# Performance work log

Measured on AMD Instinct MI355X. Metric: run time of the kernel, lower is better.

The kernel has to match this reference:

```python
import jax, jax.numpy as jnp
import numpy as np

LOG_STD2 = float(np.log(0.001))  # matches nn.init posterior_W_u/v fill, unused: params are random here


def _mvg_layer(x, M, u, v, eps):
    # append ones column (bias trick): [B, in] -> [B, in+1]
    x1 = jnp.concatenate([x, jnp.ones((x.shape[0], 1), x.dtype)], axis=1)
    # W = M + diag(exp(.5u)) @ eps @ diag(exp(.5v))  ==  M + row/col scaled eps
    W = M + jnp.exp(0.5 * u)[:, None] * eps * jnp.exp(0.5 * v)[None, :]
    return x1 @ W


def setup_inputs() -> dict:
    key = jax.random.key(0)
    ks = jax.random.split(key, 17)
    dims = [(2049, 4096), (4097, 4096), (4097, 4096), (4097, 2048)]
    inp = {"x": jax.random.normal(ks[0], (8192, 2048), dtype=jnp.float32)}
    ki = 1
    for i, (fin, fout) in enumerate(dims):
        inp[f"M{i}"] = jax.random.normal(ks[ki], (fin, fout), dtype=jnp.float32) * 0.001; ki += 1
        inp[f"u{i}"] = jax.random.normal(ks[ki], (fin,), dtype=jnp.float32) + LOG_STD2; ki += 1
        inp[f"v{i}"] = jax.random.normal(ks[ki], (fout,), dtype=jnp.float32) + LOG_STD2; ki += 1
        inp[f"eps{i}"] = jax.random.normal(ks[ki], (fin, fout), dtype=jnp.float32); ki += 1
    return inp


def reference(x, M0, u0, v0, eps0, M1, u1, v1, eps1, M2, u2, v2, eps2, M3, u3, v3, eps3):
    h = _mvg_layer(x, M0, u0, v0, eps0)
    h = _mvg_layer(jax.nn.relu(h), M1, u1, v1, eps1)
    h = _mvg_layer(jax.nn.relu(h), M2, u2, v2, eps2)
    h = _mvg_layer(jax.nn.relu(h), M3, u3, v3, eps3)
    return h
```

## Files before the change

kernel.cpp:

```cpp
#include <hip/hip_runtime.h>
#include <cstdint>
#include <cstddef>

typedef __bf16 bf16_t;
typedef __attribute__((ext_vector_type(8))) __bf16 bf16x8;
typedef __attribute__((ext_vector_type(4))) __bf16 bf16x4;
typedef __attribute__((ext_vector_type(4))) float floatx4;

__device__ __forceinline__ void cp16(const void* g, void* l) {
  __builtin_amdgcn_global_load_lds(
      (const __attribute__((address_space(1))) void*)(uintptr_t)g,
      (__attribute__((address_space(3))) void*)(uintptr_t)l, 16, 0, 0);
}

__global__ void cvt_to_bf16(const float4* __restrict__ in,
                            bf16x4* __restrict__ out, int n4) {
  int i = blockIdx.x * 256 + threadIdx.x;
  if (i < n4) {
    float4 f = in[i];
    bf16x4 o;
    o[0] = (bf16_t)f.x; o[1] = (bf16_t)f.y; o[2] = (bf16_t)f.z; o[3] = (bf16_t)f.w;
    out[i] = o;
  }
}

__global__ void prep_wt(const float* __restrict__ M, const float* __restrict__ u,
                        const float* __restrict__ v, const float* __restrict__ eps,
                        bf16_t* __restrict__ Wt, int K, int N) {
  __shared__ float tile[32][33];
  const int nb = blockIdx.x * 32, kb = blockIdx.y * 32;
  const int tx = threadIdx.x, ty = threadIdx.y;
  const float sv = __expf(0.5f * v[nb + tx]);
#pragma unroll
  for (int r = 0; r < 4; ++r) {
    const int k = kb + ty + 8 * r;
    const float su = __expf(0.5f * u[k]);
    const size_t idx = (size_t)k * N + nb + tx;
    tile[ty + 8 * r][tx] = M[idx] + su * eps[idx] * sv;
  }
  __syncthreads();
#pragma unroll
  for (int r = 0; r < 4; ++r) {
    const int n = nb + ty + 8 * r;
    Wt[(size_t)n * K + kb + tx] = (bf16_t)tile[tx][ty + 8 * r];
  }
}

__global__ void prep_bias(const float* __restrict__ M, const float* __restrict__ u,
                          const float* __restrict__ v, const float* __restrict__ eps,
                          float* __restrict__ bias, int K, int N) {
  int n = blockIdx.x * 256 + threadIdx.x;
  if (n < N) {
    const size_t idx = (size_t)K * N + n;
    bias[n] = M[idx] + __expf(0.5f * u[K]) * eps[idx] * __expf(0.5f * v[n]);
  }
}

template <int EPI>
__global__ __launch_bounds__(256, 2) void gemm_bt(
    const bf16_t* __restrict__ A, const bf16_t* __restrict__ Bt,
    const float* __restrict__ bias, void* __restrict__ Cout, int N, int K) {
  __shared__ bf16_t As[128 * 32];
  __shared__ bf16_t Bs[128 * 32];

  const int tid = threadIdx.x;
  const int lane = tid & 63;
  const int wave = tid >> 6;
  const int wm = (wave >> 1) * 64;
  const int wn = (wave & 1) * 64;
  const int bm = blockIdx.y * 128;
  const int bn = blockIdx.x * 128;

  const int srow = tid >> 2;
  const int scol = (tid & 3) * 8;
  const bf16_t* aG0 = A + (size_t)(bm + srow) * K + scol;
  const bf16_t* aG1 = aG0 + (size_t)64 * K;
  const bf16_t* bG0 = Bt + (size_t)(bn + srow) * K + scol;
  const bf16_t* bG1 = bG0 + (size_t)64 * K;
  char* aL0 = (char*)As + tid * 16;
  char* aL1 = aL0 + 4096;
  char* bL0 = (char*)Bs + tid * 16;
  char* bL1 = bL0 + 4096;

  floatx4 acc[4][4] = {};

  const int mRow = wm + (lane & 15);
  const int nRow = wn + (lane & 15);
  const int kq = lane >> 4;

  for (int k0 = 0; k0 < K; k0 += 32) {
    cp16(aG0 + k0, aL0);
    cp16(aG1 + k0, aL1);
    cp16(bG0 + k0, bL0);
    cp16(bG1 + k0, bL1);
    __syncthreads();

    const bf16x8* As8 = (const bf16x8*)As;
    const bf16x8* Bs8 = (const bf16x8*)Bs;
    bf16x8 af[4], bfr[4];
#pragma unroll
    for (int i = 0; i < 4; ++i) af[i] = As8[(mRow + i * 16) * 4 + kq];
#pragma unroll
    for (int j = 0; j < 4; ++j) bfr[j] = Bs8[(nRow + j * 16) * 4 + kq];
#pragma unroll
    for (int i = 0; i < 4; ++i)
#pragma unroll
      for (int j = 0; j < 4; ++j)
        acc[i][j] = __builtin_amdgcn_mfma_f32_16x16x32_bf16(af[i], bfr[j],
                                                            acc[i][j], 0, 0, 0);
    __syncthreads();
  }

  const int col = bn + wn + (lane & 15);
  const int row0 = bm + wm + kq * 4;
#pragma unroll
  for (int j = 0; j < 4; ++j) {
    const float bj = bias[col + j * 16];
#pragma unroll
    for (int i = 0; i < 4; ++i) {
#pragma unroll
      for (int r = 0; r < 4; ++r) {
        float v = acc[i][j][r] + bj;
        const size_t idx = (size_t)(row0 + i * 16 + r) * N + (col + j * 16);
        if (EPI == 0) {
          v = v > 0.f ? v : 0.f;
          ((bf16_t*)Cout)[idx] = (bf16_t)v;
        } else {
          ((float*)Cout)[idx] = v;
        }
      }
    }
  }
}

extern "C" void kernel_launch(void* const* d_in, const int* in_sizes, int n_in,
                              void* d_out, int out_size, void* d_ws, size_t ws_size,
                              hipStream_t stream) {
  const float* x = (const float*)d_in[0];
  const float *Mm[4], *uu[4], *vv[4], *ee[4];
  for (int i = 0; i < 4; ++i) {
    Mm[i] = (const float*)d_in[1 + 4 * i];
    uu[i] = (const float*)d_in[2 + 4 * i];
    vv[i] = (const float*)d_in[3 + 4 * i];
    ee[i] = (const float*)d_in[4 + 4 * i];
  }

  char* ws = (char*)d_ws;
  bf16_t* Wt0 = (bf16_t*)ws;
  bf16_t* Wt1 = (bf16_t*)(ws + 16777216);
  bf16_t* Wt2 = (bf16_t*)(ws + 16777216 + 33554432);
  bf16_t* Wt3 = (bf16_t*)(ws + 16777216 + 2u * 33554432);
  char* bptr = ws + 2u * 16777216 + 2u * 33554432;
  float* bias0 = (float*)(bptr);
  float* bias1 = (float*)(bptr + 16384);
  float* bias2 = (float*)(bptr + 32768);
  float* bias3 = (float*)(bptr + 49152);
  char* act = bptr + 65536;
  bf16_t* hA = (bf16_t*)act;
  bf16_t* hB = (bf16_t*)(act + 67108864);
  bf16_t* xb = (bf16_t*)d_out;

  cvt_to_bf16<<<16384, 256, 0, stream>>>((const float4*)x, (bf16x4*)xb,
                                         8192 * 2048 / 4);
  prep_wt<<<dim3(4096 / 32, 2048 / 32), dim3(32, 8), 0, stream>>>(
      Mm[0], uu[0], vv[0], ee[0], Wt0, 2048, 4096);
  prep_wt<<<dim3(4096 / 32, 4096 / 32), dim3(32, 8), 0, stream>>>(
      Mm[1], uu[1], vv[1], ee[1], Wt1, 4096, 4096);
  prep_wt<<<dim3(4096 / 32, 4096 / 32), dim3(32, 8), 0, stream>>>(
      Mm[2], uu[2], vv[2], ee[2], Wt2, 4096, 4096);
  prep_wt<<<dim3(2048 / 32, 4096 / 32), dim3(32, 8), 0, stream>>>(
      Mm[3], uu[3], vv[3], ee[3], Wt3, 4096, 2048);
  prep_bias<<<16, 256, 0, stream>>>(Mm[0], uu[0], vv[0], ee[0], bias0, 2048, 4096);
  prep_bias<<<16, 256, 0, stream>>>(Mm[1], uu[1], vv[1], ee[1], bias1, 4096, 4096);
  prep_bias<<<16, 256, 0, stream>>>(Mm[2], uu[2], vv[2], ee[2], bias2, 4096, 4096);
  prep_bias<<<8, 256, 0, stream>>>(Mm[3], uu[3], vv[3], ee[3], bias3, 4096, 2048);

  gemm_bt<0><<<dim3(32, 64), 256, 0, stream>>>(xb, Wt0, bias0, hA, 4096, 2048);
  gemm_bt<0><<<dim3(32, 64), 256, 0, stream>>>(hA, Wt1, bias1, hB, 4096, 4096);
  gemm_bt<0><<<dim3(32, 64), 256, 0, stream>>>(hB, Wt2, bias2, hA, 4096, 4096);
  gemm_bt<1><<<dim3(16, 64), 256, 0, stream>>>(hA, Wt3, bias3, d_out, 2048, 4096);
}
```

Before: 1.317 ms.

## Replace 128x128 GEMM with 256x256 double-buffered pipelined bf16 MFMA kernel

Replaces the simple single-buffered 128x128 tile GEMM with a 512-thread 256x256 tile kernel. It uses a 64-deep K step, double-buffered dynamic LDS (128 KB), and XOR-swizzled LDS layout to avoid bank conflicts. Global-to-LDS prefetch of the next tiles is interleaved with MFMA phases using sched barriers and setprio, and a block-id remap improves L2 locality. This removes the per-iteration full sync stalls and low arithmetic intensity of the old kernel, at the cost of high register and LDS use that limits occupancy, plus intricate waitcnt logic that is easy to get wrong.

```diff
diff --git a/kernel.cpp b/kernel.cpp
--- a/kernel.cpp
+++ b/kernel.cpp
@@ -11,6 +11,12 @@
   __builtin_amdgcn_global_load_lds(
       (const __attribute__((address_space(1))) void*)(uintptr_t)g,
       (__attribute__((address_space(3))) void*)(uintptr_t)l, 16, 0, 0);
+}
+
+__device__ __forceinline__ void stage_half(const bf16_t* p, int K, char* dst,
+                                           int tid) {
+  cp16(p, dst + tid * 16);
+  cp16(p + (size_t)128 * K, dst + 8192 + tid * 16);
 }
 
 __global__ void cvt_to_bf16(const float4* __restrict__ in,
@@ -56,72 +62,160 @@
   }
 }
 
+template <int CURB>
+__device__ __forceinline__ void ktile(int t, int NT, int K,
+                                      const bf16_t* gA, const bf16_t* gB,
+                                      char* lds, int tid, int aoff0, int boff0,
+                                      floatx4 (&acc)[8][4]) {
+  constexpr int curO = CURB * 65536;
+  constexpr int nxtO = (CURB ^ 1) * 65536;
+  bf16x8 af[4], bb[4];
+
+#pragma unroll
+  for (int m = 0; m < 4; ++m)
+    af[m] = *(const bf16x8*)(lds + curO + aoff0 + m * 1024);
+#pragma unroll
+  for (int n = 0; n < 4; ++n)
+    bb[n] = *(const bf16x8*)(lds + curO + 32768 + boff0 + n * 1024);
+  if (t + 1 < NT)
+    stage_half(gA + (size_t)(t + 1) * 64 + 32, K, lds + nxtO + 16384, tid);
+  __builtin_amdgcn_s_barrier();
+  asm volatile("s_waitcnt lgkmcnt(0)" ::: "memory");
+  __builtin_amdgcn_sched_barrier(0);
+  __builtin_amdgcn_s_setprio(1);
+#pragma unroll
+  for (int m = 0; m < 4; ++m)
+#pragma unroll
+    for (int n = 0; n < 4; ++n)
+      acc[m][n] = __builtin_amdgcn_mfma_f32_16x16x32_bf16(af[m], bb[n],
+                                                          acc[m][n], 0, 0, 0);
+  __builtin_amdgcn_s_setprio(0);
+  __builtin_amdgcn_sched_barrier(0);
+  __builtin_amdgcn_s_barrier();
+
+#pragma unroll
+  for (int m = 0; m < 4; ++m)
+    af[m] = *(const bf16x8*)(lds + curO + aoff0 + (m + 4) * 1024);
+  if (t + 1 < NT)
+    stage_half(gB + (size_t)(t + 1) * 64 + 32, K, lds + nxtO + 49152, tid);
+  __builtin_amdgcn_s_barrier();
+  asm volatile("s_waitcnt lgkmcnt(0)" ::: "memory");
+  __builtin_amdgcn_sched_barrier(0);
+  __builtin_amdgcn_s_setprio(1);
+#pragma unroll
+  for (int m = 0; m < 4; ++m)
+#pragma unroll
+    for (int n = 0; n < 4; ++n)
+      acc[m + 4][n] = __builtin_amdgcn_mfma_f32_16x16x32_bf16(af[m], bb[n],
+                                                              acc[m + 4][n], 0, 0, 0);
+  __builtin_amdgcn_s_setprio(0);
+  __builtin_amdgcn_sched_barrier(0);
+  __builtin_amdgcn_s_barrier();
+
+#pragma unroll
+  for (int m = 0; m < 4; ++m)
+    af[m] = *(const bf16x8*)(lds + curO + 16384 + aoff0 + m * 1024);
+#pragma unroll
+  for (int n = 0; n < 4; ++n)
+    bb[n] = *(const bf16x8*)(lds + curO + 49152 + boff0 + n * 1024);
+  if (t + 2 < NT)
+    stage_half(gA + (size_t)(t + 2) * 64, K, lds + curO, tid);
+  __builtin_amdgcn_s_barrier();
+  asm volatile("s_waitcnt lgkmcnt(0)" ::: "memory");
+  __builtin_amdgcn_sched_barrier(0);
+  __builtin_amdgcn_s_setprio(1);
+#pragma unroll
+  for (int m = 0; m < 4; ++m)
+#pragma unroll
+    for (int n = 0; n < 4; ++n)
+      acc[m][n] = __builtin_amdgcn_mfma_f32_16x16x32_bf16(af[m], bb[n],
+                                                          acc[m][n], 0, 0, 0);
+  __builtin_amdgcn_s_setprio(0);
+  __builtin_amdgcn_sched_barrier(0);
+  __builtin_amdgcn_s_barrier();
+
+#pragma unroll
+  for (int m = 0; m < 4; ++m)
+    af[m] = *(const bf16x8*)(lds + curO + 16384 + aoff0 + (m + 4) * 1024);
+  if (t + 2 < NT)
+    stage_half(gB + (size_t)(t + 2) * 64, K, lds + curO + 32768, tid);
+  __builtin_amdgcn_s_barrier();
+  asm volatile("s_waitcnt lgkmcnt(0)" ::: "memory");
+  __builtin_amdgcn_sched_barrier(0);
+  __builtin_amdgcn_s_setprio(1);
+#pragma unroll
+  for (int m = 0; m < 4; ++m)
+#pragma unroll
+    for (int n = 0; n < 4; ++n)
+      acc[m + 4][n] = __builtin_amdgcn_mfma_f32_16x16x32_bf16(af[m], bb[n],
+                                                              acc[m + 4][n], 0, 0, 0);
+  __builtin_amdgcn_s_setprio(0);
+  __builtin_amdgcn_sched_barrier(0);
+  if (t + 2 < NT) {
+    asm volatile("s_waitcnt vmcnt(4)" ::: "memory");
+  } else if (t + 1 < NT) {
+    asm volatile("s_waitcnt vmcnt(0)" ::: "memory");
+  }
+  __builtin_amdgcn_s_barrier();
+}
+
 template <int EPI>
-__global__ __launch_bounds__(256, 2) void gemm_bt(
+__global__ __launch_bounds__(512, 2) void gemm256(
     const bf16_t* __restrict__ A, const bf16_t* __restrict__ Bt,
     const float* __restrict__ bias, void* __restrict__ Cout, int N, int K) {
-  __shared__ bf16_t As[128 * 32];
-  __shared__ bf16_t Bs[128 * 32];
-
+  extern __shared__ char lds[];
   const int tid = threadIdx.x;
   const int lane = tid & 63;
   const int wave = tid >> 6;
-  const int wm = (wave >> 1) * 64;
-  const int wn = (wave & 1) * 64;
-  const int bm = blockIdx.y * 128;
-  const int bn = blockIdx.x * 128;
+  const int wm = (wave >> 2) * 128;
+  const int wn = (wave & 3) * 64;
+  const int l15 = lane & 15;
+  const int kqs = ((lane >> 4) ^ ((lane >> 1) & 3)) << 4;
+  const int aoff0 = (wm + l15) * 64 + kqs;
+  const int bofB0 = (wn + l15) * 64 + kqs;
+
+  const int gx = gridDim.x;
+  int id = blockIdx.y * gx + blockIdx.x;
+  const int cpx = (gx * (int)gridDim.y) >> 3;
+  id = (id & 7) * cpx + (id >> 3);
+  const int bm = (id / gx) * 256;
+  const int bn = (id % gx) * 256;
 
   const int srow = tid >> 2;
-  const int scol = (tid & 3) * 8;
-  const bf16_t* aG0 = A + (size_t)(bm + srow) * K + scol;
-  const bf16_t* aG1 = aG0 + (size_t)64 * K;
-  const bf16_t* bG0 = Bt + (size_t)(bn + srow) * K + scol;
-  const bf16_t* bG1 = bG0 + (size_t)64 * K;
-  char* aL0 = (char*)As + tid * 16;
-  char* aL1 = aL0 + 4096;
-  char* bL0 = (char*)Bs + tid * 16;
-  char* bL1 = bL0 + 4096;
-
-  floatx4 acc[4][4] = {};
-
-  const int mRow = wm + (lane & 15);
-  const int nRow = wn + (lane & 15);
-  const int kq = lane >> 4;
-
-  for (int k0 = 0; k0 < K; k0 += 32) {
-    cp16(aG0 + k0, aL0);
-    cp16(aG1 + k0, aL1);
-    cp16(bG0 + k0, bL0);
-    cp16(bG1 + k0, bL1);
-    __syncthreads();
-
-    const bf16x8* As8 = (const bf16x8*)As;
-    const bf16x8* Bs8 = (const bf16x8*)Bs;
-    bf16x8 af[4], bfr[4];
-#pragma unroll
-    for (int i = 0; i < 4; ++i) af[i] = As8[(mRow + i * 16) * 4 + kq];
-#pragma unroll
-    for (int j = 0; j < 4; ++j) bfr[j] = Bs8[(nRow + j * 16) * 4 + kq];
-#pragma unroll
-    for (int i = 0; i < 4; ++i)
-#pragma unroll
-      for (int j = 0; j < 4; ++j)
-        acc[i][j] = __builtin_amdgcn_mfma_f32_16x16x32_bf16(af[i], bfr[j],
-                                                            acc[i][j], 0, 0, 0);
-    __syncthreads();
-  }
-
-  const int col = bn + wn + (lane & 15);
-  const int row0 = bm + wm + kq * 4;
+  const int ss8 = ((tid & 3) ^ ((tid >> 3) & 3)) * 8;
+  const bf16_t* gA = A + (size_t)(bm + srow) * K + ss8;
+  const bf16_t* gB = Bt + (size_t)(bn + srow) * K + ss8;
+
+  const int NT = K >> 6;
+
+  floatx4 acc[8][4] = {};
+
+  stage_half(gA, K, lds + 0, tid);
+  stage_half(gA + 32, K, lds + 16384, tid);
+  stage_half(gB, K, lds + 32768, tid);
+  stage_half(gB + 32, K, lds + 49152, tid);
+  stage_half(gA + 64, K, lds + 65536, tid);
+  stage_half(gB + 64, K, lds + 65536 + 32768, tid);
+  asm volatile("s_waitcnt vmcnt(4)" ::: "memory");
+  __builtin_amdgcn_s_barrier();
+
+  for (int t = 0; t < NT; t += 2) {
+    ktile<0>(t, NT, K, gA, gB, lds, tid, aoff0, bofB0, acc);
+    ktile<1>(t + 1, NT, K, gA, gB, lds, tid, aoff0, bofB0, acc);
+  }
+
+  const int kq4 = lane >> 4;
+  const int col0 = bn + wn + l15;
+  const int row0 = bm + wm + kq4 * 4;
 #pragma unroll
   for (int j = 0; j < 4; ++j) {
-    const float bj = bias[col + j * 16];
-#pragma unroll
-    for (int i = 0; i < 4; ++i) {
+    const float bj = bias[col0 + j * 16];
+#pragma unroll
+    for (int m = 0; m < 8; ++m) {
 #pragma unroll
       for (int r = 0; r < 4; ++r) {
-        float v = acc[i][j][r] + bj;
-        const size_t idx = (size_t)(row0 + i * 16 + r) * N + (col + j * 16);
+        float v = acc[m][j][r] + bj;
+        const size_t idx = (size_t)(row0 + m * 16 + r) * N + (col0 + j * 16);
         if (EPI == 0) {
           v = v > 0.f ? v : 0.f;
           ((bf16_t*)Cout)[idx] = (bf16_t)v;
@@ -160,6 +254,15 @@
   bf16_t* hB = (bf16_t*)(act + 67108864);
   bf16_t* xb = (bf16_t*)d_out;
 
+  static bool attr_set = false;
+  if (!attr_set) {
+    (void)hipFuncSetAttribute(reinterpret_cast<const void*>(&gemm256<0>),
+                              hipFuncAttributeMaxDynamicSharedMemorySize, 131072);
+    (void)hipFuncSetAttribute(reinterpret_cast<const void*>(&gemm256<1>),
+                              hipFuncAttributeMaxDynamicSharedMemorySize, 131072);
+    attr_set = true;
+  }
+
   cvt_to_bf16<<<16384, 256, 0, stream>>>((const float4*)x, (bf16x4*)xb,
                                          8192 * 2048 / 4);
   prep_wt<<<dim3(4096 / 32, 2048 / 32), dim3(32, 8), 0, stream>>>(
@@ -175,8 +278,8 @@
   prep_bias<<<16, 256, 0, stream>>>(Mm[2], uu[2], vv[2], ee[2], bias2, 4096, 4096);
   prep_bias<<<8, 256, 0, stream>>>(Mm[3], uu[3], vv[3], ee[3], bias3, 4096, 2048);
 
-  gemm_bt<0><<<dim3(32, 64), 256, 0, stream>>>(xb, Wt0, bias0, hA, 4096, 2048);
-  gemm_bt<0><<<dim3(32, 64), 256, 0, stream>>>(hA, Wt1, bias1, hB, 4096, 4096);
-  gemm_bt<0><<<dim3(32, 64), 256, 0, stream>>>(hB, Wt2, bias2, hA, 4096, 4096);
-  gemm_bt<1><<<dim3(16, 64), 256, 0, stream>>>(hA, Wt3, bias3, d_out, 2048, 4096);
-}
+  gemm256<0><<<dim3(16, 32), 512, 131072, stream>>>(xb, Wt0, bias0, hA, 4096, 2048);
+  gemm256<0><<<dim3(16, 32), 512, 131072, stream>>>(hA, Wt1, bias1, hB, 4096, 4096);
+  gemm256<0><<<dim3(16, 32), 512, 131072, stream>>>(hB, Wt2, bias2, hA, 4096, 4096);
+  gemm256<1><<<dim3(8, 32), 512, 131072, stream>>>(hA, Wt3, bias3, d_out, 2048, 4096);
+}
```

New measurement: 1.171 ms. 1.12x faster.
